# Kernel tuning notes

Measured on AMD Instinct MI355X. Metric: run time of the kernel, lower is better.

## Reference

```python
import jax, jax.numpy as jnp
import numpy as np

EPS = 1e-5

def _conv1x1(x, w, b):
    # x: (B,C,H,W), w: (O,C), b: (O,)
    return jnp.einsum('bchw,oc->bohw', x, w) + b[None, :, None, None]

def _maxpool2(x):
    B, C, H, W = x.shape
    return x.reshape(B, C, H // 2, 2, W // 2, 2).max(axis=(3, 5))

def setup_inputs() -> dict:
    key = jax.random.key(0)
    ks = jax.random.split(key, 12)
    B, C, Ci, H, W = 8, 256, 128, 64, 64
    s = lambda k, shape, scale: jax.random.normal(k, shape, jnp.float32) * scale
    return {
        'x': s(ks[0], (B, C, H, W), 1.0),
        'neighborFeat': s(ks[1], (B, C, H, W), 1.0),
        'g_w': s(ks[2], (Ci, C), 0.05), 'g_b': jnp.zeros((Ci,), jnp.float32),
        'theta_w': s(ks[3], (Ci, C), 0.05), 'theta_b': jnp.zeros((Ci,), jnp.float32),
        'phi_w': s(ks[4], (Ci, C), 0.05), 'phi_b': jnp.zeros((Ci,), jnp.float32),
        'w_w': s(ks[5], (C, Ci), 0.05), 'w_b': jnp.zeros((C,), jnp.float32),
        'bn_gamma': s(ks[6], (C,), 0.1) + 1.0,
        'bn_beta': s(ks[7], (C,), 0.1),
        'bn_mean': s(ks[8], (C,), 0.1),
        'bn_var': jax.random.uniform(ks[9], (C,), jnp.float32, 0.5, 1.5),
    }

def reference(x, neighborFeat, g_w, g_b, theta_w, theta_b, phi_w, phi_b,
              w_w, w_b, bn_gamma, bn_beta, bn_mean, bn_var):
    B, C, H, W = x.shape
    Ci = g_w.shape[0]
    # g: conv1x1 on x then maxpool2 -> (B, Nkv, Ci)
    g_x = _maxpool2(_conv1x1(x, g_w, g_b)).reshape(B, Ci, -1).transpose(0, 2, 1)
    # theta: conv1x1 on neighborFeat, full res -> (B, Nq, Ci)
    theta_x = _conv1x1(neighborFeat, theta_w, theta_b).reshape(B, Ci, -1).transpose(0, 2, 1)
    # phi: conv1x1 on neighborFeat then maxpool2 -> (B, Ci, Nkv)
    phi_x = _maxpool2(_conv1x1(neighborFeat, phi_w, phi_b)).reshape(B, Ci, -1)
    f = jnp.einsum('bqc,bck->bqk', theta_x, phi_x)       # (B, Nq, Nkv)
    f_div_C = jax.nn.softmax(f, axis=-1)
    y = jnp.einsum('bqk,bkc->bqc', f_div_C, g_x)          # (B, Nq, Ci)
    y = y.transpose(0, 2, 1).reshape(B, Ci, H, W)
    # W: conv1x1 + BatchNorm (eval mode with running stats)
    wy = _conv1x1(y, w_w, w_b)
    wy = (wy - bn_mean[None, :, None, None]) * (bn_gamma[None, :, None, None]
          * jax.lax.rsqrt(bn_var + EPS)[None, :, None, None]) + bn_beta[None, :, None, None]
    return wy + x
```

## Files before the change

### kernel.cpp

```cpp
#include <hip/hip_runtime.h>

typedef __attribute__((ext_vector_type(8))) short short8;
typedef __attribute__((ext_vector_type(4))) short short4v;
typedef __attribute__((ext_vector_type(4))) float f32x4;
typedef __attribute__((ext_vector_type(16))) float f32x16;
typedef __attribute__((ext_vector_type(4))) unsigned u32x4;

#define LOG2E 1.4426950408889634f

__device__ __forceinline__ float bf2f(short s) {
  union { unsigned u; float f; } cv;
  cv.u = ((unsigned)(unsigned short)s) << 16;
  return cv.f;
}
__device__ __forceinline__ short f2bf(float f) {
  union { float f; unsigned u; } cv;
  cv.f = f;
  unsigned r = (cv.u + 0x7fffu + ((cv.u >> 16) & 1u)) >> 16;
  return (short)(unsigned short)r;
}
__device__ __forceinline__ unsigned cvtpk(float a, float b) {
  unsigned r;
  asm("v_cvt_pk_bf16_f32 %0, %1, %2" : "=v"(r) : "v"(a), "v"(b));
  return r;
}
__device__ __forceinline__ float fexp2(float x) {
  float r;
  asm("v_exp_f32 %0, %1" : "=v"(r) : "v"(x));
  return r;
}
__device__ __forceinline__ void load_lds16(const void* g, void* l) {
  __builtin_amdgcn_global_load_lds(
      (const __attribute__((address_space(1))) void*)g,
      (__attribute__((address_space(3))) void*)l, 16, 0, 0);
}

#define MFMA16(a, b, c) __builtin_amdgcn_mfma_f32_16x16x32_bf16((a), (b), (c), 0, 0, 0)
#define MFMA32(a, b, c) __builtin_amdgcn_mfma_f32_32x32x16_bf16((a), (b), (c), 0, 0, 0)

__global__ __launch_bounds__(256) void cvt_w(
    const float* __restrict__ s0, const float* __restrict__ s1,
    const float* __restrict__ s2, const float* __restrict__ s3,
    short* __restrict__ d)
{
  const float* srcs[4] = {s0, s1, s2, s3};
  const float* s = srcs[blockIdx.y];
  int i = (blockIdx.x * 256 + threadIdx.x) * 4;
  f32x4 v = *reinterpret_cast<const f32x4*>(s + i);
  short4v o;
  #pragma unroll
  for (int j = 0; j < 4; j++) o[j] = f2bf(v[j]);
  *reinterpret_cast<short4v*>(d + (size_t)blockIdx.y * 32768 + i) = o;
}

template <int NPROJ, int MODE1>
__device__ __forceinline__ void conv_body(
    short (*in_t)[40], short (*wt)[40],
    const float* __restrict__ in,
    const short* __restrict__ w0, const float* __restrict__ bias0,
    const short* __restrict__ w1, const float* __restrict__ bias1,
    short* __restrict__ out0, short* __restrict__ out1)
{
  const int b = blockIdx.y;
  const int p0 = blockIdx.x * 128;
  const int tid = threadIdx.x;
  const int wave = tid >> 6, lane = tid & 63;
  const int lr = lane & 15, lg = lane >> 4;

  const short* wsrc[2] = {w0, w1};

  f32x4 acc[NPROJ][8];
  #pragma unroll
  for (int pj = 0; pj < NPROJ; pj++)
    #pragma unroll
    for (int n = 0; n < 8; n++) acc[pj][n] = (f32x4)0.0f;

  for (int kc = 0; kc < 256; kc += 32) {
    __syncthreads();
    {
      int c = tid >> 4;
      int pg = (tid & 15) * 8;
      const float* src = in + ((size_t)(b * 256 + kc + c)) * 4096 + p0 + pg;
      f32x4 v0 = *reinterpret_cast<const f32x4*>(src);
      f32x4 v1 = *reinterpret_cast<const f32x4*>(src + 4);
      #pragma unroll
      for (int j = 0; j < 8; j++) {
        int p = pg + j;
        int a = ((p & 63) >> 1) * 4 + ((p >> 6) << 1) + (p & 1);
        float fv = (j < 4) ? v0[j] : v1[j - 4];
        in_t[a][c ^ ((((a >> 3) & 3)) << 3)] = f2bf(fv);
      }
    }
    if (tid < NPROJ * 128) {
      int pj = tid >> 7, o = tid & 127;
      const short8* src = reinterpret_cast<const short8*>(wsrc[pj] + (size_t)o * 256 + kc);
      int f = (o >> 3) & 3;
      #pragma unroll
      for (int gq = 0; gq < 4; gq++)
        *reinterpret_cast<short8*>(&wt[pj * 128 + o][(gq ^ f) * 8]) = src[gq];
    }
    __syncthreads();

    int arow = wave * 16 + lr;
    short8 afrag = *reinterpret_cast<const short8*>(
        &in_t[arow][(lg ^ ((arow >> 3) & 3)) * 8]);
    #pragma unroll
    for (int pj = 0; pj < NPROJ; pj++) {
      #pragma unroll
      for (int n = 0; n < 8; n++) {
        int brow = n * 16 + lr;
        short8 bfrag = *reinterpret_cast<const short8*>(
            &wt[pj * 128 + brow][(lg ^ ((brow >> 3) & 3)) * 8]);
        acc[pj][n] = MFMA16(afrag, bfrag, acc[pj][n]);
      }
    }
  }

  const float* bsrc[2] = {bias0, bias1};
  short* osrc[2] = {out0, out1};
  const int kp = blockIdx.x * 32 + wave * 4 + lg;
  #pragma unroll
  for (int pj = 0; pj < NPROJ; pj++) {
    const int mode = (pj == 0 && NPROJ == 2) ? 0 : MODE1;
    #pragma unroll
    for (int n = 0; n < 8; n++) {
      int o = n * 16 + lr;
      float bv = bsrc[pj][o];
      if (mode == 0) {
        #pragma unroll
        for (int r = 0; r < 4; r++) {
          int pix = (wave * 4 + lg) * 2 + (r & 1) + ((r >> 1) & 1) * 64;
          osrc[pj][((size_t)b * 4096 + p0 + pix) * 128 + o] =
              f2bf((acc[pj][n][r] + bv) * LOG2E);
        }
      } else {
        f32x4 v = acc[pj][n];
        float pv = fmaxf(fmaxf(v[0], v[1]), fmaxf(v[2], v[3])) + bv;
        if (mode == 1)
          osrc[pj][((size_t)b * 1024 + kp) * 128 + o] = f2bf(pv);
        else
          osrc[pj][((size_t)b * 128 + o) * 1024 + kp] = f2bf(pv);
      }
    }
  }
}

__global__ __launch_bounds__(512, 4) void conv_all(
    const float* __restrict__ nb, const float* __restrict__ x,
    const short* __restrict__ th_w, const float* __restrict__ th_b,
    const short* __restrict__ ph_w, const float* __restrict__ ph_b,
    const short* __restrict__ g_w, const float* __restrict__ g_b,
    short* __restrict__ theta, short* __restrict__ phi_kc,
    short* __restrict__ g_ck)
{
  __shared__ short in_t[128][40];
  __shared__ short wt[256][40];
  if (blockIdx.z == 0)
    conv_body<2, 1>(in_t, wt, nb, th_w, th_b, ph_w, ph_b, theta, phi_kc);
  else
    conv_body<1, 2>(in_t, wt, x, g_w, g_b, nullptr, nullptr, g_ck, nullptr);
}

__global__ __launch_bounds__(512) void attn_wconv(
    const short* __restrict__ theta, const short* __restrict__ phi,
    const short* __restrict__ g, const short* __restrict__ ww,
    const float* __restrict__ wb,
    const float* __restrict__ gamma, const float* __restrict__ beta,
    const float* __restrict__ mean, const float* __restrict__ var,
    const float* __restrict__ x, float* __restrict__ out)
{
  __shared__ char lds[131072];
  __shared__ float ml[8][32][2];

  const int b = blockIdx.y;
  const int q0 = blockIdx.x * 128;
  const int tid = threadIdx.x;
  const int wave = tid >> 6, lane = tid & 63;
  const int l31 = lane & 31, hi = lane >> 5;
  const int zw = wave >> 2, wq = wave & 3;

  short8 ath[8];
  {
    const short* tq = theta + ((size_t)b * 4096 + q0 + wq * 32 + l31) * 128 + hi * 8;
    #pragma unroll
    for (int s = 0; s < 8; s++)
      ath[s] = *reinterpret_cast<const short8*>(tq + s * 16);
  }

  const short* psrc[4];
  {
    int rb = wq * 16 + (lane >> 4), sl = lane & 15;
    #pragma unroll
    for (int i = 0; i < 4; i++) {
      int r = rb + i * 4;
      psrc[i] = phi + ((size_t)b * 1024 + zw * 512 + r) * 128 + ((sl ^ (r & 15)) * 8);
    }
  }
  const short* gsrc[4];
  {
    int rb = wq * 32 + (lane >> 3), sl = lane & 7;
    #pragma unroll
    for (int i = 0; i < 4; i++) {
      int r = rb + i * 8;
      gsrc[i] = g + ((size_t)b * 128 + r) * 1024 + zw * 512 + ((sl ^ (r & 7)) * 8);
    }
  }

  float mrun = -1e30f, lpart = 0.0f;
  f32x16 acc[4];
  #pragma unroll
  for (int n = 0; n < 4; n++) acc[n] = (f32x16)0.0f;

  {
    char* pb = lds + zw * 16384 + wq * 4096;
    char* gb = lds + 65536 + zw * 16384 + wq * 4096;
    #pragma unroll
    for (int i = 0; i < 4; i++) {
      load_lds16(psrc[i], pb + i * 1024);
      load_lds16(gsrc[i], gb + i * 1024);
    }
  }

  for (int t = 0; t < 8; t++) {
    __syncthreads();
    char* pb = lds + ((t & 1) * 2 + zw) * 16384;
    char* gb = lds + 65536 + ((t & 1) * 2 + zw) * 16384;

    if (t < 7) {
      char* pb2 = lds + (((t + 1) & 1) * 2 + zw) * 16384 + wq * 4096;
      char* gb2 = lds + 65536 + (((t + 1) & 1) * 2 + zw) * 16384 + wq * 4096;
      #pragma unroll
      for (int i = 0; i < 4; i++) {
        load_lds16(psrc[i] + (t + 1) * 8192, pb2 + i * 1024);
        load_lds16(gsrc[i] + (t + 1) * 64, gb2 + i * 1024);
      }
    }

    f32x16 facc0 = (f32x16)0.0f, facc1 = (f32x16)0.0f;
    __builtin_amdgcn_s_setprio(1);
    #pragma unroll
    for (int s = 0; s < 8; s++) {
      int slot = (s << 1) | hi;
      short8 pf0 = *reinterpret_cast<const short8*>(
          pb + l31 * 256 + ((slot ^ (l31 & 15)) * 16));
      short8 pf1 = *reinterpret_cast<const short8*>(
          pb + (32 + l31) * 256 + ((slot ^ (l31 & 15)) * 16));
      facc0 = MFMA32(pf0, ath[s], facc0);
      facc1 = MFMA32(pf1, ath[s], facc1);
    }
    __builtin_amdgcn_s_setprio(0);

    float mv[16];
    #pragma unroll
    for (int r = 0; r < 16; r++) mv[r] = fmaxf(facc0[r], facc1[r]);
    #pragma unroll
    for (int s = 8; s >= 1; s >>= 1)
      #pragma unroll
      for (int r = 0; r < s; r++) mv[r] = fmaxf(mv[r], mv[r + s]);
    float m = fmaxf(mv[0], __shfl_xor(mv[0], 32));

    if (__any(m - mrun > 14.0f)) {
      float mn = fmaxf(mrun, m);
      float sc = fexp2(mrun - mn);
      mrun = mn;
      lpart *= sc;
      #pragma unroll
      for (int reg = 0; reg < 16; reg++) {
        int qr = (reg & 3) + 8 * (reg >> 2) + 4 * hi;
        float sr = __shfl(sc, qr);
        #pragma unroll
        for (int n = 0; n < 4; n++) acc[n][reg] *= sr;
      }
    }
    #pragma unroll
    for (int r = 0; r < 16; r++) facc0[r] = fexp2(facc0[r] - mrun);
    #pragma unroll
    for (int r = 0; r < 16; r++) facc1[r] = fexp2(facc1[r] - mrun);
    {
      float sv[16];
      #pragma unroll
      for (int r = 0; r < 16; r++) sv[r] = facc0[r] + facc1[r];
      #pragma unroll
      for (int s = 8; s >= 1; s >>= 1)
        #pragma unroll
        for (int r = 0; r < s; r++) sv[r] += sv[r + s];
      lpart += sv[0];
    }

    __builtin_amdgcn_s_setprio(1);
    #pragma unroll
    for (int s = 0; s < 4; s++) {
      const int base = (s & 1) * 8;
      float p0, p1, p2, p3, p4, p5, p6, p7;
      if (s < 2) {
        p0 = facc0[base + 0]; p1 = facc0[base + 1]; p2 = facc0[base + 2]; p3 = facc0[base + 3];
        p4 = facc0[base + 4]; p5 = facc0[base + 5]; p6 = facc0[base + 6]; p7 = facc0[base + 7];
      } else {
        p0 = facc1[base + 0]; p1 = facc1[base + 1]; p2 = facc1[base + 2]; p3 = facc1[base + 3];
        p4 = facc1[base + 4]; p5 = facc1[base + 5]; p6 = facc1[base + 6]; p7 = facc1[base + 7];
      }
      unsigned P0w0 = cvtpk(p0, p1), P0w1 = cvtpk(p2, p3);
      unsigned P1w0 = cvtpk(p4, p5), P1w1 = cvtpk(p6, p7);
      unsigned x0 = (unsigned)__shfl_xor((int)P0w0, 32);
      unsigned x1 = (unsigned)__shfl_xor((int)P0w1, 32);
      unsigned y0 = (unsigned)__shfl_xor((int)P1w0, 32);
      unsigned y1 = (unsigned)__shfl_xor((int)P1w1, 32);
      union { u32x4 u; short8 s8; } pf;
      pf.u[0] = hi ? y0 : P0w0;
      pf.u[1] = hi ? y1 : P0w1;
      pf.u[2] = hi ? P1w0 : x0;
      pf.u[3] = hi ? P1w1 : x1;
      int slot = (s << 1) | hi;
      #pragma unroll
      for (int n = 0; n < 4; n++) {
        int rg = n * 32 + l31;
        short8 gf = *reinterpret_cast<const short8*>(
            gb + rg * 128 + ((slot ^ (rg & 7)) * 16));
        acc[n] = MFMA32(pf.s8, gf, acc[n]);
      }
    }
    __builtin_amdgcn_s_setprio(0);
  }

  float lsum = lpart + __shfl_xor(lpart, 32);
  if (lane < 32) { ml[wave][l31][0] = mrun; ml[wave][l31][1] = lsum; }
  __syncthreads();

  float* sc_s = (float*)(lds + 114688);
  float* sh_s = (float*)(lds + 118784);
  if (tid < 256) {
    float s = gamma[tid] * rsqrtf(var[tid] + 1e-5f);
    sc_s[tid] = s;
    sh_s[tid] = (wb[tid] - mean[tid]) * s + beta[tid];
  }

  float mo = ml[wave ^ 4][l31][0];
  float lo = ml[wave ^ 4][l31][1];
  float M = fmaxf(mrun, mo);
  float e0 = fexp2(mrun - M), e1 = fexp2(mo - M);
  float wown = e0 / (e0 * lsum + e1 * lo);
  #pragma unroll
  for (int reg = 0; reg < 16; reg++) {
    int qr = (reg & 3) + 8 * (reg >> 2) + 4 * hi;
    float wr = __shfl(wown, qr);
    #pragma unroll
    for (int n = 0; n < 4; n++) acc[n][reg] *= wr;
  }
  float* mb = (float*)(lds + wq * 16384);
  if (zw == 1) {
    #pragma unroll
    for (int n = 0; n < 4; n++)
      #pragma unroll
      for (int reg = 0; reg < 16; reg++) {
        int qrow = (reg & 3) + 8 * (reg >> 2) + 4 * hi;
        mb[qrow * 128 + n * 32 + l31] = acc[n][reg];
      }
  }
  __syncthreads();
  short* y_s = (short*)(lds + 65536);
  if (zw == 0) {
    #pragma unroll
    for (int n = 0; n < 4; n++)
      #pragma unroll
      for (int reg = 0; reg < 16; reg++) {
        int qrow = (reg & 3) + 8 * (reg >> 2) + 4 * hi;
        float v = acc[n][reg] + mb[qrow * 128 + n * 32 + l31];
        y_s[(wq * 32 + qrow) * 136 + n * 32 + l31] = f2bf(v);
      }
  }
  __syncthreads();

  const int lr = lane & 15, lg = lane >> 4;
  f32x4 acc2[2][8];
  #pragma unroll
  for (int mm = 0; mm < 2; mm++)
    #pragma unroll
    for (int n = 0; n < 8; n++) acc2[mm][n] = (f32x4)0.0f;

  #pragma unroll
  for (int kk = 0; kk < 4; kk++) {
    short8 af[2], bfr[8];
    #pragma unroll
    for (int mm = 0; mm < 2; mm++)
      af[mm] = *reinterpret_cast<const short8*>(
          ww + (size_t)(wave * 32 + mm * 16 + lr) * 128 + kk * 32 + lg * 8);
    #pragma unroll
    for (int n = 0; n < 8; n++)
      bfr[n] = *reinterpret_cast<const short8*>(
          &y_s[(n * 16 + lr) * 136 + kk * 32 + lg * 8]);
    #pragma unroll
    for (int mm = 0; mm < 2; mm++)
      #pragma unroll
      for (int n = 0; n < 8; n++)
        acc2[mm][n] = MFMA16(af[mm], bfr[n], acc2[mm][n]);
  }

  #pragma unroll
  for (int mm = 0; mm < 2; mm++) {
    #pragma unroll
    for (int n = 0; n < 8; n++) {
      #pragma unroll
      for (int r = 0; r < 4; r++) {
        int co = wave * 32 + mm * 16 + lg * 4 + r;
        int q = q0 + n * 16 + lr;
        size_t oidx = ((size_t)b * 256 + co) * 4096 + q;
        float v = acc2[mm][n][r] * sc_s[co] + sh_s[co];
        out[oidx] = v + x[oidx];
      }
    }
  }
}

extern "C" void kernel_launch(void* const* d_in, const int* in_sizes, int n_in,
                              void* d_out, int out_size, void* d_ws, size_t ws_size,
                              hipStream_t stream)
{
  const float* x    = (const float*)d_in[0];
  const float* nb   = (const float*)d_in[1];
  const float* g_w  = (const float*)d_in[2];
  const float* g_b  = (const float*)d_in[3];
  const float* th_w = (const float*)d_in[4];
  const float* th_b = (const float*)d_in[5];
  const float* ph_w = (const float*)d_in[6];
  const float* ph_b = (const float*)d_in[7];
  const float* w_w  = (const float*)d_in[8];
  const float* w_b  = (const float*)d_in[9];
  const float* gam  = (const float*)d_in[10];
  const float* bet  = (const float*)d_in[11];
  const float* mu   = (const float*)d_in[12];
  const float* var  = (const float*)d_in[13];
  float* out = (float*)d_out;

  char* ws = (char*)d_ws;
  short* theta_full = (short*)(ws);
  short* phi_kc     = (short*)(ws + (size_t)(8u << 20));
  short* g_ck       = (short*)(ws + (size_t)(10u << 20));
  short* wts        = (short*)(ws + (size_t)(12u << 20));
  short* th_wb = wts;
  short* ph_wb = wts + 32768;
  short* g_wb  = wts + 2 * 32768;
  short* w_wb  = wts + 3 * 32768;

  cvt_w<<<dim3(32, 4), 256, 0, stream>>>(th_w, ph_w, g_w, w_w, wts);
  conv_all<<<dim3(32, 8, 2), 512, 0, stream>>>(nb, x, th_wb, th_b, ph_wb, ph_b,
                                               g_wb, g_b, theta_full, phi_kc, g_ck);
  attn_wconv<<<dim3(32, 8), 512, 0, stream>>>(theta_full, phi_kc, g_ck, w_wb, w_b,
                                              gam, bet, mu, var, x, out);
}
```

Measured before the change: 74.68 us.

## Split attention KV range across four wave groups with 1024-thread blocks

Doubles the attention block from 8 to 16 waves, so each of four wave groups handles a quarter of the key range per tile instead of a half. The per-wave score tile shrinks to one 32x32 MFMA, and partial softmax states from the four groups are merged through LDS in a two-stage reduction. The output conv is split so each wave produces 16 output channels. The aim is more waves in flight to hide latency with fewer registers per wave, at the cost of extra barriers, more reduction traffic through LDS, and smaller MFMA batches per tile.

```diff
diff --git a/kernel.cpp b/kernel.cpp
--- a/kernel.cpp
+++ b/kernel.cpp
@@ -161,7 +161,7 @@
     conv_body<1, 2>(in_t, wt, x, g_w, g_b, nullptr, nullptr, g_ck, nullptr);
 }
 
-__global__ __launch_bounds__(512) void attn_wconv(
+__global__ __launch_bounds__(1024, 4) void attn_wconv(
     const short* __restrict__ theta, const short* __restrict__ phi,
     const short* __restrict__ g, const short* __restrict__ ww,
     const float* __restrict__ wb,
@@ -170,7 +170,9 @@
     const float* __restrict__ x, float* __restrict__ out)
 {
   __shared__ char lds[131072];
-  __shared__ float ml[8][32][2];
+  __shared__ float ml[16][32][2];
+  __shared__ float sc_s[256];
+  __shared__ float sh_s[256];
 
   const int b = blockIdx.y;
   const int q0 = blockIdx.x * 128;
@@ -187,22 +189,22 @@
       ath[s] = *reinterpret_cast<const short8*>(tq + s * 16);
   }
 
-  const short* psrc[4];
+  const short* psrc[2];
   {
-    int rb = wq * 16 + (lane >> 4), sl = lane & 15;
-    #pragma unroll
-    for (int i = 0; i < 4; i++) {
-      int r = rb + i * 4;
-      psrc[i] = phi + ((size_t)b * 1024 + zw * 512 + r) * 128 + ((sl ^ (r & 15)) * 8);
-    }
-  }
-  const short* gsrc[4];
+    int r0 = wq * 8 + (lane >> 4), sl = lane & 15;
+    #pragma unroll
+    for (int i = 0; i < 2; i++) {
+      int r = r0 + i * 4;
+      psrc[i] = phi + ((size_t)b * 1024 + zw * 256 + r) * 128 + ((sl ^ (r & 15)) * 8);
+    }
+  }
+  const short* gsrc[2];
   {
-    int rb = wq * 32 + (lane >> 3), sl = lane & 7;
-    #pragma unroll
-    for (int i = 0; i < 4; i++) {
-      int r = rb + i * 8;
-      gsrc[i] = g + ((size_t)b * 128 + r) * 1024 + zw * 512 + ((sl ^ (r & 7)) * 8);
+    int r0 = wq * 32 + (lane >> 2), sl = lane & 3;
+    #pragma unroll
+    for (int i = 0; i < 2; i++) {
+      int r = r0 + i * 16;
+      gsrc[i] = g + ((size_t)b * 128 + r) * 1024 + zw * 256 + ((sl ^ (r & 3)) * 8);
     }
   }
 
@@ -212,10 +214,10 @@
   for (int n = 0; n < 4; n++) acc[n] = (f32x16)0.0f;
 
   {
-    char* pb = lds + zw * 16384 + wq * 4096;
-    char* gb = lds + 65536 + zw * 16384 + wq * 4096;
-    #pragma unroll
-    for (int i = 0; i < 4; i++) {
+    char* pb = lds + zw * 8192 + wq * 2048;
+    char* gb = lds + 65536 + zw * 8192 + wq * 2048;
+    #pragma unroll
+    for (int i = 0; i < 2; i++) {
       load_lds16(psrc[i], pb + i * 1024);
       load_lds16(gsrc[i], gb + i * 1024);
     }
@@ -223,38 +225,35 @@
 
   for (int t = 0; t < 8; t++) {
     __syncthreads();
-    char* pb = lds + ((t & 1) * 2 + zw) * 16384;
-    char* gb = lds + 65536 + ((t & 1) * 2 + zw) * 16384;
+    char* pb = lds + ((t & 1) * 4 + zw) * 8192;
+    char* gb = lds + 65536 + ((t & 1) * 4 + zw) * 8192;
 
     if (t < 7) {
-      char* pb2 = lds + (((t + 1) & 1) * 2 + zw) * 16384 + wq * 4096;
-      char* gb2 = lds + 65536 + (((t + 1) & 1) * 2 + zw) * 16384 + wq * 4096;
-      #pragma unroll
-      for (int i = 0; i < 4; i++) {
-        load_lds16(psrc[i] + (t + 1) * 8192, pb2 + i * 1024);
-        load_lds16(gsrc[i] + (t + 1) * 64, gb2 + i * 1024);
-      }
-    }
-
-    f32x16 facc0 = (f32x16)0.0f, facc1 = (f32x16)0.0f;
+      char* pb2 = lds + (((t + 1) & 1) * 4 + zw) * 8192 + wq * 2048;
+      char* gb2 = lds + 65536 + (((t + 1) & 1) * 4 + zw) * 8192 + wq * 2048;
+      #pragma unroll
+      for (int i = 0; i < 2; i++) {
+        load_lds16(psrc[i] + (t + 1) * 4096, pb2 + i * 1024);
+        load_lds16(gsrc[i] + (t + 1) * 32, gb2 + i * 1024);
+      }
+    }
+
+    f32x16 facc = (f32x16)0.0f;
     __builtin_amdgcn_s_setprio(1);
     #pragma unroll
     for (int s = 0; s < 8; s++) {
       int slot = (s << 1) | hi;
-      short8 pf0 = *reinterpret_cast<const short8*>(
+      short8 pf = *reinterpret_cast<const short8*>(
           pb + l31 * 256 + ((slot ^ (l31 & 15)) * 16));
-      short8 pf1 = *reinterpret_cast<const short8*>(
-          pb + (32 + l31) * 256 + ((slot ^ (l31 & 15)) * 16));
-      facc0 = MFMA32(pf0, ath[s], facc0);
-      facc1 = MFMA32(pf1, ath[s], facc1);
+      facc = MFMA32(pf, ath[s], facc);
     }
     __builtin_amdgcn_s_setprio(0);
 
-    float mv[16];
-    #pragma unroll
-    for (int r = 0; r < 16; r++) mv[r] = fmaxf(facc0[r], facc1[r]);
-    #pragma unroll
-    for (int s = 8; s >= 1; s >>= 1)
+    float mv[8];
+    #pragma unroll
+    for (int r = 0; r < 8; r++) mv[r] = fmaxf(facc[r], facc[r + 8]);
+    #pragma unroll
+    for (int s = 4; s >= 1; s >>= 1)
       #pragma unroll
       for (int r = 0; r < s; r++) mv[r] = fmaxf(mv[r], mv[r + s]);
     float m = fmaxf(mv[0], __shfl_xor(mv[0], 32));
@@ -273,15 +272,13 @@
       }
     }
     #pragma unroll
-    for (int r = 0; r < 16; r++) facc0[r] = fexp2(facc0[r] - mrun);
-    #pragma unroll
-    for (int r = 0; r < 16; r++) facc1[r] = fexp2(facc1[r] - mrun);
+    for (int r = 0; r < 16; r++) facc[r] = fexp2(facc[r] - mrun);
     {
-      float sv[16];
-      #pragma unroll
-      for (int r = 0; r < 16; r++) sv[r] = facc0[r] + facc1[r];
-      #pragma unroll
-      for (int s = 8; s >= 1; s >>= 1)
+      float sv[8];
+      #pragma unroll
+      for (int r = 0; r < 8; r++) sv[r] = facc[r] + facc[r + 8];
+      #pragma unroll
+      for (int s = 4; s >= 1; s >>= 1)
         #pragma unroll
         for (int r = 0; r < s; r++) sv[r] += sv[r + s];
       lpart += sv[0];
@@ -289,18 +286,12 @@
 
     __builtin_amdgcn_s_setprio(1);
     #pragma unroll
-    for (int s = 0; s < 4; s++) {
-      const int base = (s & 1) * 8;
-      float p0, p1, p2, p3, p4, p5, p6, p7;
-      if (s < 2) {
-        p0 = facc0[base + 0]; p1 = facc0[base + 1]; p2 = facc0[base + 2]; p3 = facc0[base + 3];
-        p4 = facc0[base + 4]; p5 = facc0[base + 5]; p6 = facc0[base + 6]; p7 = facc0[base + 7];
-      } else {
-        p0 = facc1[base + 0]; p1 = facc1[base + 1]; p2 = facc1[base + 2]; p3 = facc1[base + 3];
-        p4 = facc1[base + 4]; p5 = facc1[base + 5]; p6 = facc1[base + 6]; p7 = facc1[base + 7];
-      }
-      unsigned P0w0 = cvtpk(p0, p1), P0w1 = cvtpk(p2, p3);
-      unsigned P1w0 = cvtpk(p4, p5), P1w1 = cvtpk(p6, p7);
+    for (int s = 0; s < 2; s++) {
+      const int base = s * 8;
+      unsigned P0w0 = cvtpk(facc[base + 0], facc[base + 1]);
+      unsigned P0w1 = cvtpk(facc[base + 2], facc[base + 3]);
+      unsigned P1w0 = cvtpk(facc[base + 4], facc[base + 5]);
+      unsigned P1w1 = cvtpk(facc[base + 6], facc[base + 7]);
       unsigned x0 = (unsigned)__shfl_xor((int)P0w0, 32);
       unsigned x1 = (unsigned)__shfl_xor((int)P0w1, 32);
       unsigned y0 = (unsigned)__shfl_xor((int)P1w0, 32);
@@ -315,7 +306,7 @@
       for (int n = 0; n < 4; n++) {
         int rg = n * 32 + l31;
         short8 gf = *reinterpret_cast<const short8*>(
-            gb + rg * 128 + ((slot ^ (rg & 7)) * 16));
+            gb + rg * 64 + ((slot ^ (rg & 3)) * 16));
         acc[n] = MFMA32(pf.s8, gf, acc[n]);
       }
     }
@@ -324,89 +315,104 @@
 
   float lsum = lpart + __shfl_xor(lpart, 32);
   if (lane < 32) { ml[wave][l31][0] = mrun; ml[wave][l31][1] = lsum; }
-  __syncthreads();
-
-  float* sc_s = (float*)(lds + 114688);
-  float* sh_s = (float*)(lds + 118784);
   if (tid < 256) {
     float s = gamma[tid] * rsqrtf(var[tid] + 1e-5f);
     sc_s[tid] = s;
     sh_s[tid] = (wb[tid] - mean[tid]) * s + beta[tid];
   }
-
-  float mo = ml[wave ^ 4][l31][0];
-  float lo = ml[wave ^ 4][l31][1];
-  float M = fmaxf(mrun, mo);
-  float e0 = fexp2(mrun - M), e1 = fexp2(mo - M);
-  float wown = e0 / (e0 * lsum + e1 * lo);
-  #pragma unroll
-  for (int reg = 0; reg < 16; reg++) {
-    int qr = (reg & 3) + 8 * (reg >> 2) + 4 * hi;
-    float wr = __shfl(wown, qr);
-    #pragma unroll
-    for (int n = 0; n < 4; n++) acc[n][reg] *= wr;
-  }
-  float* mb = (float*)(lds + wq * 16384);
-  if (zw == 1) {
+  __syncthreads();
+
+  {
+    float m0 = ml[wq][l31][0],      l0 = ml[wq][l31][1];
+    float m1 = ml[4 + wq][l31][0],  l1 = ml[4 + wq][l31][1];
+    float m2 = ml[8 + wq][l31][0],  l2 = ml[8 + wq][l31][1];
+    float m3 = ml[12 + wq][l31][0], l3 = ml[12 + wq][l31][1];
+    float M = fmaxf(fmaxf(m0, m1), fmaxf(m2, m3));
+    float L = fexp2(m0 - M) * l0 + fexp2(m1 - M) * l1 +
+              fexp2(m2 - M) * l2 + fexp2(m3 - M) * l3;
+    float wown = fexp2(mrun - M) / L;
+    #pragma unroll
+    for (int reg = 0; reg < 16; reg++) {
+      int qr = (reg & 3) + 8 * (reg >> 2) + 4 * hi;
+      float wr = __shfl(wown, qr);
+      #pragma unroll
+      for (int n = 0; n < 4; n++) acc[n][reg] *= wr;
+    }
+  }
+
+  float* bufA = (float*)lds;
+  float* bufB = (float*)(lds + 65536);
+  if (zw == 1 || zw == 3) {
+    float* dst = (zw == 1) ? bufA : bufB;
     #pragma unroll
     for (int n = 0; n < 4; n++)
       #pragma unroll
       for (int reg = 0; reg < 16; reg++) {
         int qrow = (reg & 3) + 8 * (reg >> 2) + 4 * hi;
-        mb[qrow * 128 + n * 32 + l31] = acc[n][reg];
+        dst[(wq * 32 + qrow) * 128 + n * 32 + l31] = acc[n][reg];
       }
   }
   __syncthreads();
-  short* y_s = (short*)(lds + 65536);
   if (zw == 0) {
     #pragma unroll
     for (int n = 0; n < 4; n++)
       #pragma unroll
       for (int reg = 0; reg < 16; reg++) {
         int qrow = (reg & 3) + 8 * (reg >> 2) + 4 * hi;
-        float v = acc[n][reg] + mb[qrow * 128 + n * 32 + l31];
+        acc[n][reg] += bufA[(wq * 32 + qrow) * 128 + n * 32 + l31];
+      }
+  } else if (zw == 2) {
+    #pragma unroll
+    for (int n = 0; n < 4; n++)
+      #pragma unroll
+      for (int reg = 0; reg < 16; reg++) {
+        int qrow = (reg & 3) + 8 * (reg >> 2) + 4 * hi;
+        int idx = (wq * 32 + qrow) * 128 + n * 32 + l31;
+        bufB[idx] += acc[n][reg];
+      }
+  }
+  __syncthreads();
+  short* y_s = (short*)lds;
+  if (zw == 0) {
+    #pragma unroll
+    for (int n = 0; n < 4; n++)
+      #pragma unroll
+      for (int reg = 0; reg < 16; reg++) {
+        int qrow = (reg & 3) + 8 * (reg >> 2) + 4 * hi;
+        float v = acc[n][reg] + bufB[(wq * 32 + qrow) * 128 + n * 32 + l31];
         y_s[(wq * 32 + qrow) * 136 + n * 32 + l31] = f2bf(v);
       }
   }
   __syncthreads();
 
   const int lr = lane & 15, lg = lane >> 4;
-  f32x4 acc2[2][8];
-  #pragma unroll
-  for (int mm = 0; mm < 2; mm++)
-    #pragma unroll
-    for (int n = 0; n < 8; n++) acc2[mm][n] = (f32x4)0.0f;
+  f32x4 acc2[8];
+  #pragma unroll
+  for (int n = 0; n < 8; n++) acc2[n] = (f32x4)0.0f;
 
   #pragma unroll
   for (int kk = 0; kk < 4; kk++) {
-    short8 af[2], bfr[8];
-    #pragma unroll
-    for (int mm = 0; mm < 2; mm++)
-      af[mm] = *reinterpret_cast<const short8*>(
-          ww + (size_t)(wave * 32 + mm * 16 + lr) * 128 + kk * 32 + lg * 8);
+    short8 af = *reinterpret_cast<const short8*>(
+        ww + (size_t)(wave * 16 + lr) * 128 + kk * 32 + lg * 8);
+    short8 bfr[8];
     #pragma unroll
     for (int n = 0; n < 8; n++)
       bfr[n] = *reinterpret_cast<const short8*>(
           &y_s[(n * 16 + lr) * 136 + kk * 32 + lg * 8]);
     #pragma unroll
-    for (int mm = 0; mm < 2; mm++)
-      #pragma unroll
-      for (int n = 0; n < 8; n++)
-        acc2[mm][n] = MFMA16(af[mm], bfr[n], acc2[mm][n]);
-  }
-
-  #pragma unroll
-  for (int mm = 0; mm < 2; mm++) {
-    #pragma unroll
-    for (int n = 0; n < 8; n++) {
-      #pragma unroll
-      for (int r = 0; r < 4; r++) {
-        int co = wave * 32 + mm * 16 + lg * 4 + r;
-        int q = q0 + n * 16 + lr;
-        size_t oidx = ((size_t)b * 256 + co) * 4096 + q;
-        float v = acc2[mm][n][r] * sc_s[co] + sh_s[co];
-        out[oidx] = v + x[oidx];
-      }
+    for (int n = 0; n < 8; n++)
+      acc2[n] = MFMA16(af, bfr[n], acc2[n]);
+  }
+
+  #pragma unroll
+  for (int n = 0; n < 8; n++) {
+    #pragma unroll
+    for (int r = 0; r < 4; r++) {
+      int co = wave * 16 + lg * 4 + r;
+      int q = q0 + n * 16 + lr;
+      size_t oidx = ((size_t)b * 256 + co) * 4096 + q;
+      float v = acc2[n][r] * sc_s[co] + sh_s[co];
+      out[oidx] = v + x[oidx];
     }
   }
 }
@@ -444,6 +450,6 @@
   cvt_w<<<dim3(32, 4), 256, 0, stream>>>(th_w, ph_w, g_w, w_w, wts);
   conv_all<<<dim3(32, 8, 2), 512, 0, stream>>>(nb, x, th_wb, th_b, ph_wb, ph_b,
                                                g_wb, g_b, theta_full, phi_kc, g_ck);
-  attn_wconv<<<dim3(32, 8), 512, 0, stream>>>(theta_full, phi_kc, g_ck, w_wb, w_b,
-                                              gam, bet, mu, var, x, out);
-}
+  attn_wconv<<<dim3(32, 8), 1024, 0, stream>>>(theta_full, phi_kc, g_ck, w_wb, w_b,
+                                               gam, bet, mu, var, x, out);
+}
```

After: 126.8 us. 69.8% more time.
